# Kernel tuning notes

Hardware: AMD Instinct MI355X
Metric: run time of the kernel (lower is better)

Reference implementation:

```python
import jax, jax.numpy as jnp
import numpy as np

B, S, H, NUM_P = 32, 1024, 768, 49
P2 = NUM_P * 2


def setup_inputs() -> dict:
    key = jax.random.key(0)
    ks = jax.random.split(key, 8)
    hidden_states = jax.random.normal(ks[0], (B, S, H), dtype=jnp.float32)
    batch_subject_ids = jax.random.randint(ks[1], (B, 2), 0, S, dtype=jnp.int32)
    input_mask = jax.random.randint(ks[2], (B, S), 0, 2, dtype=jnp.int32)
    attn_w = jax.random.normal(ks[3], (1, H), dtype=jnp.float32) * 0.02
    attn_b = jnp.zeros((1,), dtype=jnp.float32)
    gate_w = jax.random.normal(ks[4], (H, 2 * H), dtype=jnp.float32) * 0.02
    gate_b = jnp.zeros((H,), dtype=jnp.float32)
    lin_w = jax.random.normal(ks[5], (P2, H), dtype=jnp.float32) * 0.02
    lin_b = jnp.zeros((P2,), dtype=jnp.float32)
    return {
        'hidden_states': hidden_states,
        'batch_subject_ids': batch_subject_ids,
        'input_mask': input_mask,
        'attn_w': attn_w,
        'attn_b': attn_b,
        'gate_w': gate_w,
        'gate_b': gate_b,
        'lin_w': lin_w,
        'lin_b': lin_b,
    }


def reference(hidden_states, batch_subject_ids, input_mask, attn_w, attn_b,
              gate_w, gate_b, lin_w, lin_b):
    # NOTE: the torch module computes s = h[s_start] + h[s_end] from
    # batch_subject_ids but never uses it -> dead code, omitted.
    # Dropout(p=0.4) is treated in eval mode (identity).
    b, s, h = hidden_states.shape
    # cue_len per batch, clamped to [1, S] as in the torch code
    cue_len = jnp.clip(jnp.sum(input_mask, axis=-1), 1, s)            # [B]
    valid = jnp.arange(s)[None, :] < cue_len[:, None]                 # [B,S] bool

    # attention pooling over the first cue_len tokens
    scores = jnp.einsum('bsh,oh->bso', hidden_states, attn_w) + attn_b  # [B,S,1]
    scores = jnp.where(valid[..., None], scores, -jnp.inf)
    attn = jax.nn.softmax(scores, axis=1)                             # [B,S,1]
    s_x = jnp.sum(attn * hidden_states, axis=1)                       # [B,H]

    # gate(cat([s_x, h_i])) split into the two halves of gate_w
    gate_ws = gate_w[:, :h]   # acts on s_x
    gate_wh = gate_w[:, h:]   # acts on h_i
    g_logit = (jnp.einsum('bh,oh->bo', s_x, gate_ws)[:, None, :]
               + jnp.einsum('bsh,oh->bso', hidden_states, gate_wh)
               + gate_b)                                              # [B,S,H]
    g = jax.nn.sigmoid(g_logit)
    fused = g * s_x[:, None, :] + (1.0 - g) * hidden_states           # [B,S,H]
    all_s = jnp.where(valid[..., None], fused, 0.0)                   # zeros beyond cue_len

    hs = hidden_states + all_s
    out = jax.nn.sigmoid(jnp.einsum('bsh,oh->bso', hs, lin_w) + lin_b)
    eps = 1e-7
    return jnp.clip(out, eps, 1.0 - eps)                              # [B,S,2*num_p]
```

## Files before the change

kernel.cpp:

```cpp
#include <hip/hip_runtime.h>
#include <hip/hip_bf16.h>
#include <cstdint>

#define NB 32
#define NS 1024
#define NH 768
#define NP 98

typedef __attribute__((ext_vector_type(8))) short short8;
typedef __attribute__((ext_vector_type(4))) float f32x4;

static __device__ __forceinline__ ushort f2bf(float f) {
  uint32_t u = __builtin_bit_cast(uint32_t, f);
  u += 0x7fff + ((u >> 16) & 1);
  return (ushort)(u >> 16);
}
static __device__ __forceinline__ float bf2f(ushort h) {
  uint32_t u = ((uint32_t)h) << 16;
  return __builtin_bit_cast(float, u);
}
static __device__ __forceinline__ void gload16(const ushort* g, ushort* l) {
  __builtin_amdgcn_global_load_lds((const __attribute__((address_space(1))) uint32_t*)g,
                                   (__attribute__((address_space(3))) uint32_t*)l, 16, 0, 0);
}

__global__ void k_wprep(const float* __restrict__ gate_w, const float* __restrict__ lin_w,
                        ushort* __restrict__ wh_bf, ushort* __restrict__ gs_bf,
                        ushort* __restrict__ lin_bf) {
  int r = blockIdx.x, t = threadIdx.x;
  if (r < NH) {
    float4 v = *(const float4*)(gate_w + (size_t)r * (2 * NH) + NH + t * 4);
    ushort4 h;
    h.x = f2bf(v.x); h.y = f2bf(v.y); h.z = f2bf(v.z); h.w = f2bf(v.w);
    *(ushort4*)&wh_bf[(size_t)r * NH + t * 4] = h;
  } else if (r < 2 * NH) {
    int n = r - NH;
    float4 v = *(const float4*)(gate_w + (size_t)n * (2 * NH) + t * 4);
    ushort4 h;
    h.x = f2bf(v.x); h.y = f2bf(v.y); h.z = f2bf(v.z); h.w = f2bf(v.w);
    *(ushort4*)&gs_bf[(size_t)n * NH + t * 4] = h;
  } else {
    int n = r - 2 * NH;
    ushort4 h; h.x = 0; h.y = 0; h.z = 0; h.w = 0;
    if (n < NP) {
      float4 v = *(const float4*)(lin_w + (size_t)n * NH + t * 4);
      h.x = f2bf(v.x); h.y = f2bf(v.y); h.z = f2bf(v.z); h.w = f2bf(v.w);
    }
    *(ushort4*)&lin_bf[(size_t)n * NH + t * 4] = h;
  }
}

__global__ void k_prep(const float* __restrict__ hidden, const float* __restrict__ aw,
                       const float* __restrict__ ab, ushort* __restrict__ hid_bf,
                       float* __restrict__ scores) {
  int wid = threadIdx.x >> 6, lane = threadIdx.x & 63;
  int rbase = blockIdx.x * 32 + wid * 8;
  float w0[12];
#pragma unroll
  for (int j = 0; j < 3; ++j) {
    float4 wv = *(const float4*)(aw + j * 256 + lane * 4);
    w0[4 * j] = wv.x; w0[4 * j + 1] = wv.y; w0[4 * j + 2] = wv.z; w0[4 * j + 3] = wv.w;
  }
  float abv = ab[0];
  for (int r = rbase; r < rbase + 8; ++r) {
    const float* row = hidden + (size_t)r * NH;
    float acc = 0.f;
#pragma unroll
    for (int j = 0; j < 3; ++j) {
      float4 v = *(const float4*)(row + j * 256 + lane * 4);
      acc += v.x * w0[4 * j] + v.y * w0[4 * j + 1] + v.z * w0[4 * j + 2] + v.w * w0[4 * j + 3];
      ushort4 h;
      h.x = f2bf(v.x); h.y = f2bf(v.y); h.z = f2bf(v.z); h.w = f2bf(v.w);
      *(ushort4*)&hid_bf[(size_t)r * NH + j * 256 + lane * 4] = h;
    }
#pragma unroll
    for (int off = 32; off; off >>= 1) acc += __shfl_xor(acc, off);
    if (lane == 0) scores[r] = acc + abv;
  }
}

__global__ void k_stats(const int* __restrict__ mask, const float* __restrict__ scores,
                        int* __restrict__ cue, float* __restrict__ mout,
                        float* __restrict__ lout) {
  int b = blockIdx.x, t = threadIdx.x;
  int lane = t & 63, w = t >> 6;
  __shared__ float red[4];
  __shared__ int redi[4];
  __shared__ int cue_s;

  int sm = 0;
#pragma unroll
  for (int i = 0; i < 4; ++i) sm += mask[b * NS + t + 256 * i];
#pragma unroll
  for (int off = 32; off; off >>= 1) sm += __shfl_xor(sm, off);
  if (lane == 0) redi[w] = sm;
  __syncthreads();
  if (t == 0) {
    int tot = redi[0] + redi[1] + redi[2] + redi[3];
    tot = min(max(tot, 1), NS);
    cue_s = tot;
    cue[b] = tot;
  }
  __syncthreads();
  int cl = cue_s;

  float mx = -1e30f;
#pragma unroll
  for (int i = 0; i < 4; ++i) {
    int s = t + 256 * i;
    if (s < cl) mx = fmaxf(mx, scores[b * NS + s]);
  }
#pragma unroll
  for (int off = 32; off; off >>= 1) mx = fmaxf(mx, __shfl_xor(mx, off));
  if (lane == 0) red[w] = mx;
  __syncthreads();
  float m = fmaxf(fmaxf(red[0], red[1]), fmaxf(red[2], red[3]));
  __syncthreads();

  float sum = 0.f;
#pragma unroll
  for (int i = 0; i < 4; ++i) {
    int s = t + 256 * i;
    if (s < cl) sum += __expf(scores[b * NS + s] - m);
  }
#pragma unroll
  for (int off = 32; off; off >>= 1) sum += __shfl_xor(sum, off);
  if (lane == 0) red[w] = sum;
  __syncthreads();
  if (t == 0) {
    mout[b] = m;
    lout[b] = red[0] + red[1] + red[2] + red[3];
  }
}

__global__ void k_sx(const ushort* __restrict__ hid_bf, const float* __restrict__ scores,
                     const int* __restrict__ cue, const float* __restrict__ m,
                     const float* __restrict__ l, float* __restrict__ sx) {
  int b = blockIdx.y, ch = blockIdx.x, t = threadIdx.x;
  int s0 = ch * 64;
  int cl = cue[b];
  if (s0 >= cl) return;
  __shared__ float w[64];
  if (t < 64) {
    int s = s0 + t;
    float wv = 0.f;
    if (s < cl) wv = __expf(scores[b * NS + s] - m[b]) / l[b];
    w[t] = wv;
  }
  __syncthreads();
  float4 a; a.x = 0.f; a.y = 0.f; a.z = 0.f; a.w = 0.f;
  const ushort* base = hid_bf + ((size_t)(b * NS + s0)) * NH;
  for (int s = 0; s < 64; ++s) {
    float ws = w[s];
    ushort4 v = *(const ushort4*)(base + s * NH + t * 4);
    a.x = fmaf(ws, bf2f(v.x), a.x);
    a.y = fmaf(ws, bf2f(v.y), a.y);
    a.z = fmaf(ws, bf2f(v.z), a.z);
    a.w = fmaf(ws, bf2f(v.w), a.w);
  }
  float* dst = sx + b * NH + t * 4;
  atomicAdd(dst + 0, a.x);
  atomicAdd(dst + 1, a.y);
  atomicAdd(dst + 2, a.z);
  atomicAdd(dst + 3, a.w);
}

__global__ void k_g1(const float* __restrict__ sx, const ushort* __restrict__ gs_bf,
                     float* __restrict__ g1) {
  int b = blockIdx.y, og = blockIdx.x, t = threadIdx.x;
  int w = t >> 6, lane = t & 63;
  float sreg[12];
#pragma unroll
  for (int e = 0; e < 12; ++e) sreg[e] = sx[b * NH + lane * 12 + e];
#pragma unroll 4
  for (int j = 0; j < 32; ++j) {
    int o = og * 128 + w * 32 + j;
    const ushort* gr = gs_bf + (size_t)o * NH + lane * 12;
    ushort us[12];
    *(ushort4*)&us[0] = *(const ushort4*)(gr);
    *(ushort4*)&us[4] = *(const ushort4*)(gr + 4);
    *(ushort4*)&us[8] = *(const ushort4*)(gr + 8);
    float acc = 0.f;
#pragma unroll
    for (int e = 0; e < 12; ++e) acc = fmaf(bf2f(us[e]), sreg[e], acc);
#pragma unroll
    for (int off = 32; off; off >>= 1) acc += __shfl_xor(acc, off);
    if (lane == 0) g1[b * NH + o] = acc;
  }
}

__global__ __launch_bounds__(256, 3) void k_gemm1(
    const ushort* __restrict__ hid_bf, const ushort* __restrict__ wh_bf,
    const float* __restrict__ gate_b, const float* __restrict__ sx,
    const float* __restrict__ g1, const int* __restrict__ cue,
    ushort* __restrict__ hs_bf) {
  __shared__ ushort As[2][128 * 32];
  __shared__ ushort Bs[2][192 * 32];
  const int t = threadIdx.x;
  const int lane = t & 63, wid = t >> 6;
  const int half = lane >> 4, r16 = lane & 15;

  const int bid = blockIdx.x;
  const int xcd = bid & 7, i = bid >> 3;
  const int nt = i & 3, mt = xcd * 32 + (i >> 2);
  const int row0 = mt * 128, col0 = nt * 192;

  const int c0 = t, c1 = t + 256, c2 = t + 512;
  const ushort* gA0 = hid_bf + (size_t)(row0 + (c0 >> 2)) * NH + (c0 & 3) * 8;
  const ushort* gA1 = hid_bf + (size_t)(row0 + (c1 >> 2)) * NH + (c1 & 3) * 8;
  const ushort* gB0 = wh_bf + (size_t)(col0 + (c0 >> 2)) * NH + (c0 & 3) * 8;
  const ushort* gB1 = wh_bf + (size_t)(col0 + (c1 >> 2)) * NH + (c1 & 3) * 8;
  const ushort* gB2 = wh_bf + (size_t)(col0 + (c2 >> 2)) * NH + (c2 & 3) * 8;

  const int wm = wid >> 1, wn = wid & 1;
  f32x4 acc[4][6];
#pragma unroll
  for (int mf = 0; mf < 4; ++mf)
#pragma unroll
    for (int nf = 0; nf < 6; ++nf) acc[mf][nf] = (f32x4)0.f;

#define STAGE1(BUF, KS)                                  \
  {                                                      \
    const int k0_ = (KS) * 32;                           \
    gload16(gA0 + k0_, &As[BUF][c0 * 8]);                \
    gload16(gA1 + k0_, &As[BUF][c1 * 8]);                \
    gload16(gB0 + k0_, &Bs[BUF][c0 * 8]);                \
    gload16(gB1 + k0_, &Bs[BUF][c1 * 8]);                \
    gload16(gB2 + k0_, &Bs[BUF][c2 * 8]);                \
  }

#define COMPUTE1(BUF)                                                             \
  {                                                                               \
    short8 af[4], bfr[6];                                                         \
    _Pragma("unroll") for (int mf = 0; mf < 4; ++mf)                              \
        af[mf] = *(const short8*)&As[BUF][(wm * 64 + mf * 16 + r16) * 32 + half * 8]; \
    _Pragma("unroll") for (int nf = 0; nf < 6; ++nf)                              \
        bfr[nf] = *(const short8*)&Bs[BUF][(wn * 96 + nf * 16 + r16) * 32 + half * 8]; \
    _Pragma("unroll") for (int nf = 0; nf < 6; ++nf)                              \
        _Pragma("unroll") for (int mf = 0; mf < 4; ++mf)                          \
            acc[mf][nf] = __builtin_amdgcn_mfma_f32_16x16x32_bf16(af[mf], bfr[nf], \
                                                                  acc[mf][nf], 0, 0, 0); \
  }

  STAGE1(0, 0);
  __syncthreads();
#pragma unroll 1
  for (int ks2 = 0; ks2 < 12; ++ks2) {
    const int ks = ks2 * 2;
    STAGE1(1, ks + 1);
    COMPUTE1(0);
    __syncthreads();
    if (ks + 2 < 24) STAGE1(0, ks + 2);
    COMPUTE1(1);
    __syncthreads();
  }

  const int b = mt >> 3;
  const int cl = cue[b];
#pragma unroll
  for (int nf = 0; nf < 6; ++nf) {
    int col = col0 + wn * 96 + nf * 16 + r16;
    float g1v = g1[b * NH + col];
    float sxv = sx[b * NH + col];
    float gbv = gate_b[col];
#pragma unroll
    for (int mf = 0; mf < 4; ++mf) {
#pragma unroll
      for (int p = 0; p < 4; ++p) {
        int grow = row0 + wm * 64 + mf * 16 + half * 4 + p;
        float x = bf2f(hid_bf[(size_t)grow * NH + col]);
        float gl = g1v + acc[mf][nf][p] + gbv;
        float g = 1.f / (1.f + __expf(-gl));
        float fused = g * sxv + (1.f - g) * x;
        float hs = x + (((grow & 1023) < cl) ? fused : 0.f);
        hs_bf[(size_t)grow * NH + col] = f2bf(hs);
      }
    }
  }
#undef STAGE1
#undef COMPUTE1
}

__global__ __launch_bounds__(256, 4) void k_gemm2(
    const ushort* __restrict__ hs_bf, const ushort* __restrict__ lin_bf,
    const float* __restrict__ lin_b, float* __restrict__ out) {
  __shared__ ushort As[2][64 * 32];
  __shared__ ushort Bs[2][128 * 32];
  const int t = threadIdx.x;
  const int lane = t & 63, wid = t >> 6;
  const int half = lane >> 4, r16 = lane & 15;
  const int row0 = blockIdx.x * 64;

  const int cA = t;
  const int cB0 = t, cB1 = t + 256;
  const ushort* gA = hs_bf + (size_t)(row0 + (cA >> 2)) * NH + (cA & 3) * 8;
  const ushort* gB0 = lin_bf + (size_t)(cB0 >> 2) * NH + (cB0 & 3) * 8;
  const ushort* gB1 = lin_bf + (size_t)(cB1 >> 2) * NH + (cB1 & 3) * 8;

  f32x4 acc[7];
#pragma unroll
  for (int nf = 0; nf < 7; ++nf) acc[nf] = (f32x4)0.f;

#define STAGE2(BUF, KS)                                  \
  {                                                      \
    const int k0_ = (KS) * 32;                           \
    gload16(gA + k0_, &As[BUF][cA * 8]);                 \
    gload16(gB0 + k0_, &Bs[BUF][cB0 * 8]);               \
    gload16(gB1 + k0_, &Bs[BUF][cB1 * 8]);               \
  }

#define COMPUTE2(BUF)                                                          \
  {                                                                            \
    short8 a = *(const short8*)&As[BUF][(wid * 16 + r16) * 32 + half * 8];     \
    _Pragma("unroll") for (int nf = 0; nf < 7; ++nf) {                         \
      short8 bv = *(const short8*)&Bs[BUF][(nf * 16 + r16) * 32 + half * 8];   \
      acc[nf] = __builtin_amdgcn_mfma_f32_16x16x32_bf16(a, bv, acc[nf], 0, 0, 0); \
    }                                                                          \
  }

  STAGE2(0, 0);
  __syncthreads();
#pragma unroll 1
  for (int ks2 = 0; ks2 < 12; ++ks2) {
    const int ks = ks2 * 2;
    STAGE2(1, ks + 1);
    COMPUTE2(0);
    __syncthreads();
    if (ks + 2 < 24) STAGE2(0, ks + 2);
    COMPUTE2(1);
    __syncthreads();
  }

#pragma unroll
  for (int nf = 0; nf < 7; ++nf) {
    int col = nf * 16 + r16;
    bool valid = col < NP;
    float lbv = valid ? lin_b[col] : 0.f;
#pragma unroll
    for (int p = 0; p < 4; ++p) {
      int grow = row0 + wid * 16 + half * 4 + p;
      float v = acc[nf][p] + lbv;
      v = 1.f / (1.f + __expf(-v));
      v = fminf(fmaxf(v, 1e-7f), 1.f - 1e-7f);
      if (valid) out[(size_t)grow * NP + col] = v;
    }
  }
#undef STAGE2
#undef COMPUTE2
}

extern "C" void kernel_launch(void* const* d_in, const int* in_sizes, int n_in,
                              void* d_out, int out_size, void* d_ws, size_t ws_size,
                              hipStream_t stream) {
  const float* hidden = (const float*)d_in[0];
  const int* mask = (const int*)d_in[2];
  const float* attn_w = (const float*)d_in[3];
  const float* attn_b = (const float*)d_in[4];
  const float* gate_w = (const float*)d_in[5];
  const float* gate_b = (const float*)d_in[6];
  const float* lin_w = (const float*)d_in[7];
  const float* lin_b = (const float*)d_in[8];
  float* out = (float*)d_out;

  float* F = (float*)d_ws;
  int* cue = (int*)F;
  float* m = F + 32;
  float* l = F + 64;
  float* scores = F + 96;
  float* sx = scores + NB * NS;
  float* g1 = sx + NB * NH;
  ushort* wh_bf = (ushort*)(g1 + NB * NH);
  ushort* gs_bf = wh_bf + (size_t)NH * NH;
  ushort* lin_bf = gs_bf + (size_t)NH * NH;
  ushort* hid_bf = lin_bf + (size_t)128 * NH;
  ushort* hs_bf = hid_bf + (size_t)NB * NS * NH;

  hipMemsetAsync(sx, 0, NB * NH * sizeof(float), stream);
  k_wprep<<<1664, 192, 0, stream>>>(gate_w, lin_w, wh_bf, gs_bf, lin_bf);
  k_prep<<<1024, 256, 0, stream>>>(hidden, attn_w, attn_b, hid_bf, scores);
  k_stats<<<NB, 256, 0, stream>>>(mask, scores, cue, m, l);
  k_sx<<<dim3(16, NB), 192, 0, stream>>>(hid_bf, scores, cue, m, l, sx);
  k_g1<<<dim3(6, NB), 256, 0, stream>>>(sx, gs_bf, g1);
  k_gemm1<<<1024, 256, 0, stream>>>(hid_bf, wh_bf, gate_b, sx, g1, cue, hs_bf);
  k_gemm2<<<512, 256, 0, stream>>>(hs_bf, lin_bf, lin_b, out);
}
```

Baseline: 344.7 us.

## Triple-buffer GEMM pipelines with swizzled LDS and retile gemm1 to 128x128

Both GEMM kernels move from double-buffered loads with two __syncthreads per pair of k-steps to a three-stage LDS ring. Each step issues a single explicit vmcnt wait plus barrier, so global-to-LDS loads run two stages ahead of the MFMA work. An XOR swizzle on the k-quad offset is applied to both the global-load addresses and the LDS fragment reads to cut bank conflicts. gemm1 is retiled from 128x192 to 128x128 with a 1536-block grid, which lowers accumulator registers but reloads A more often. The hand-written waitcnt counts must match the number of in-flight loads exactly or the results will be wrong.

```diff
diff --git a/kernel.cpp b/kernel.cpp
--- a/kernel.cpp
+++ b/kernel.cpp
@@ -194,72 +194,79 @@
     const float* __restrict__ gate_b, const float* __restrict__ sx,
     const float* __restrict__ g1, const int* __restrict__ cue,
     ushort* __restrict__ hs_bf) {
-  __shared__ ushort As[2][128 * 32];
-  __shared__ ushort Bs[2][192 * 32];
+  __shared__ ushort As[3][128 * 32];
+  __shared__ ushort Bs[3][128 * 32];
   const int t = threadIdx.x;
   const int lane = t & 63, wid = t >> 6;
   const int half = lane >> 4, r16 = lane & 15;
 
   const int bid = blockIdx.x;
   const int xcd = bid & 7, i = bid >> 3;
-  const int nt = i & 3, mt = xcd * 32 + (i >> 2);
-  const int row0 = mt * 128, col0 = nt * 192;
-
-  const int c0 = t, c1 = t + 256, c2 = t + 512;
-  const ushort* gA0 = hid_bf + (size_t)(row0 + (c0 >> 2)) * NH + (c0 & 3) * 8;
-  const ushort* gA1 = hid_bf + (size_t)(row0 + (c1 >> 2)) * NH + (c1 & 3) * 8;
-  const ushort* gB0 = wh_bf + (size_t)(col0 + (c0 >> 2)) * NH + (c0 & 3) * 8;
-  const ushort* gB1 = wh_bf + (size_t)(col0 + (c1 >> 2)) * NH + (c1 & 3) * 8;
-  const ushort* gB2 = wh_bf + (size_t)(col0 + (c2 >> 2)) * NH + (c2 & 3) * 8;
+  const int nt = i % 6, mt = xcd * 32 + i / 6;
+  const int row0 = mt * 128, col0 = nt * 128;
+
+  const int xs = ((t >> 2) & 3) ^ ((t >> 4) & 3);
+  const int kqs = ((t & 3) ^ xs) * 8;
+  const ushort* gA0 = hid_bf + (size_t)(row0 + (t >> 2)) * NH + kqs;
+  const ushort* gA1 = hid_bf + (size_t)(row0 + 64 + (t >> 2)) * NH + kqs;
+  const ushort* gB0 = wh_bf + (size_t)(col0 + (t >> 2)) * NH + kqs;
+  const ushort* gB1 = wh_bf + (size_t)(col0 + 64 + (t >> 2)) * NH + kqs;
+  const int xr = (r16 & 3) ^ ((r16 >> 2) & 3);
 
   const int wm = wid >> 1, wn = wid & 1;
-  f32x4 acc[4][6];
+  f32x4 acc[4][4];
 #pragma unroll
   for (int mf = 0; mf < 4; ++mf)
 #pragma unroll
-    for (int nf = 0; nf < 6; ++nf) acc[mf][nf] = (f32x4)0.f;
-
-#define STAGE1(BUF, KS)                                  \
-  {                                                      \
-    const int k0_ = (KS) * 32;                           \
-    gload16(gA0 + k0_, &As[BUF][c0 * 8]);                \
-    gload16(gA1 + k0_, &As[BUF][c1 * 8]);                \
-    gload16(gB0 + k0_, &Bs[BUF][c0 * 8]);                \
-    gload16(gB1 + k0_, &Bs[BUF][c1 * 8]);                \
-    gload16(gB2 + k0_, &Bs[BUF][c2 * 8]);                \
-  }
-
-#define COMPUTE1(BUF)                                                             \
-  {                                                                               \
-    short8 af[4], bfr[6];                                                         \
-    _Pragma("unroll") for (int mf = 0; mf < 4; ++mf)                              \
-        af[mf] = *(const short8*)&As[BUF][(wm * 64 + mf * 16 + r16) * 32 + half * 8]; \
-    _Pragma("unroll") for (int nf = 0; nf < 6; ++nf)                              \
-        bfr[nf] = *(const short8*)&Bs[BUF][(wn * 96 + nf * 16 + r16) * 32 + half * 8]; \
-    _Pragma("unroll") for (int nf = 0; nf < 6; ++nf)                              \
-        _Pragma("unroll") for (int mf = 0; mf < 4; ++mf)                          \
-            acc[mf][nf] = __builtin_amdgcn_mfma_f32_16x16x32_bf16(af[mf], bfr[nf], \
+    for (int nf = 0; nf < 4; ++nf) acc[mf][nf] = (f32x4)0.f;
+
+#define STAGE1(BUF, KS)                                   \
+  {                                                       \
+    const int k0_ = (KS) * 32;                            \
+    gload16(gA0 + k0_, &As[BUF][t * 8]);                  \
+    gload16(gA1 + k0_, &As[BUF][(t + 256) * 8]);          \
+    gload16(gB0 + k0_, &Bs[BUF][t * 8]);                  \
+    gload16(gB1 + k0_, &Bs[BUF][(t + 256) * 8]);          \
+  }
+
+#define COMPUTE1(BUF)                                                               \
+  {                                                                                 \
+    short8 af[4], bfr[4];                                                           \
+    _Pragma("unroll") for (int mf = 0; mf < 4; ++mf)                                \
+        af[mf] = *(const short8*)&As[BUF][(wm * 64 + mf * 16 + r16) * 32 +          \
+                                          ((half ^ xr) * 8)];                       \
+    _Pragma("unroll") for (int nf = 0; nf < 4; ++nf)                                \
+        bfr[nf] = *(const short8*)&Bs[BUF][(wn * 64 + nf * 16 + r16) * 32 +         \
+                                           ((half ^ xr) * 8)];                      \
+    _Pragma("unroll") for (int nf = 0; nf < 4; ++nf)                                \
+        _Pragma("unroll") for (int mf = 0; mf < 4; ++mf)                            \
+            acc[mf][nf] = __builtin_amdgcn_mfma_f32_16x16x32_bf16(af[mf], bfr[nf],  \
                                                                   acc[mf][nf], 0, 0, 0); \
   }
 
+#define WAITBAR(N)                                       \
+  asm volatile("s_waitcnt vmcnt(" #N ")" ::: "memory");  \
+  __builtin_amdgcn_s_barrier();                          \
+  __builtin_amdgcn_sched_barrier(0);
+
   STAGE1(0, 0);
-  __syncthreads();
+  STAGE1(1, 1);
 #pragma unroll 1
-  for (int ks2 = 0; ks2 < 12; ++ks2) {
-    const int ks = ks2 * 2;
-    STAGE1(1, ks + 1);
-    COMPUTE1(0);
-    __syncthreads();
-    if (ks + 2 < 24) STAGE1(0, ks + 2);
-    COMPUTE1(1);
-    __syncthreads();
-  }
+  for (int tt = 0; tt < 7; ++tt) {
+    const int s0_ = tt * 3;
+    WAITBAR(4); COMPUTE1(0); STAGE1(2, s0_ + 2);
+    WAITBAR(4); COMPUTE1(1); STAGE1(0, s0_ + 3);
+    WAITBAR(4); COMPUTE1(2); STAGE1(1, s0_ + 4);
+  }
+  WAITBAR(4); COMPUTE1(0); STAGE1(2, 23);
+  WAITBAR(4); COMPUTE1(1);
+  WAITBAR(0); COMPUTE1(2);
 
   const int b = mt >> 3;
   const int cl = cue[b];
 #pragma unroll
-  for (int nf = 0; nf < 6; ++nf) {
-    int col = col0 + wn * 96 + nf * 16 + r16;
+  for (int nf = 0; nf < 4; ++nf) {
+    int col = col0 + wn * 64 + nf * 16 + r16;
     float g1v = g1[b * NH + col];
     float sxv = sx[b * NH + col];
     float gbv = gate_b[col];
@@ -284,55 +291,61 @@
 __global__ __launch_bounds__(256, 4) void k_gemm2(
     const ushort* __restrict__ hs_bf, const ushort* __restrict__ lin_bf,
     const float* __restrict__ lin_b, float* __restrict__ out) {
-  __shared__ ushort As[2][64 * 32];
-  __shared__ ushort Bs[2][128 * 32];
+  __shared__ ushort As[3][64 * 32];
+  __shared__ ushort Bs[3][128 * 32];
   const int t = threadIdx.x;
   const int lane = t & 63, wid = t >> 6;
   const int half = lane >> 4, r16 = lane & 15;
   const int row0 = blockIdx.x * 64;
 
-  const int cA = t;
-  const int cB0 = t, cB1 = t + 256;
-  const ushort* gA = hs_bf + (size_t)(row0 + (cA >> 2)) * NH + (cA & 3) * 8;
-  const ushort* gB0 = lin_bf + (size_t)(cB0 >> 2) * NH + (cB0 & 3) * 8;
-  const ushort* gB1 = lin_bf + (size_t)(cB1 >> 2) * NH + (cB1 & 3) * 8;
-
-  f32x4 acc[7];
-#pragma unroll
-  for (int nf = 0; nf < 7; ++nf) acc[nf] = (f32x4)0.f;
-
-#define STAGE2(BUF, KS)                                  \
-  {                                                      \
-    const int k0_ = (KS) * 32;                           \
-    gload16(gA + k0_, &As[BUF][cA * 8]);                 \
-    gload16(gB0 + k0_, &Bs[BUF][cB0 * 8]);               \
-    gload16(gB1 + k0_, &Bs[BUF][cB1 * 8]);               \
-  }
-
-#define COMPUTE2(BUF)                                                          \
-  {                                                                            \
-    short8 a = *(const short8*)&As[BUF][(wid * 16 + r16) * 32 + half * 8];     \
-    _Pragma("unroll") for (int nf = 0; nf < 7; ++nf) {                         \
-      short8 bv = *(const short8*)&Bs[BUF][(nf * 16 + r16) * 32 + half * 8];   \
-      acc[nf] = __builtin_amdgcn_mfma_f32_16x16x32_bf16(a, bv, acc[nf], 0, 0, 0); \
-    }                                                                          \
-  }
+  const int xs = ((t >> 2) & 3) ^ ((t >> 4) & 3);
+  const int kqs = ((t & 3) ^ xs) * 8;
+  const ushort* gA = hs_bf + (size_t)(row0 + (t >> 2)) * NH + kqs;
+  const ushort* gB0 = lin_bf + (size_t)(t >> 2) * NH + kqs;
+  const ushort* gB1 = lin_bf + (size_t)(64 + (t >> 2)) * NH + kqs;
+  const int xr = (r16 & 3) ^ ((r16 >> 2) & 3);
+
+  f32x4 acc[8];
+#pragma unroll
+  for (int nf = 0; nf < 8; ++nf) acc[nf] = (f32x4)0.f;
+
+#define STAGE2(BUF, KS)                                   \
+  {                                                       \
+    const int k0_ = (KS) * 32;                            \
+    gload16(gA + k0_, &As[BUF][t * 8]);                   \
+    gload16(gB0 + k0_, &Bs[BUF][t * 8]);                  \
+    gload16(gB1 + k0_, &Bs[BUF][(t + 256) * 8]);          \
+  }
+
+#define COMPUTE2(BUF)                                                               \
+  {                                                                                 \
+    short8 a = *(const short8*)&As[BUF][(wid * 16 + r16) * 32 + ((half ^ xr) * 8)]; \
+    _Pragma("unroll") for (int nf = 0; nf < 8; ++nf) {                              \
+      short8 bv = *(const short8*)&Bs[BUF][(nf * 16 + r16) * 32 + ((half ^ xr) * 8)]; \
+      acc[nf] = __builtin_amdgcn_mfma_f32_16x16x32_bf16(a, bv, acc[nf], 0, 0, 0);   \
+    }                                                                               \
+  }
+
+#define WAITBAR2(N)                                      \
+  asm volatile("s_waitcnt vmcnt(" #N ")" ::: "memory");  \
+  __builtin_amdgcn_s_barrier();                          \
+  __builtin_amdgcn_sched_barrier(0);
 
   STAGE2(0, 0);
-  __syncthreads();
+  STAGE2(1, 1);
 #pragma unroll 1
-  for (int ks2 = 0; ks2 < 12; ++ks2) {
-    const int ks = ks2 * 2;
-    STAGE2(1, ks + 1);
-    COMPUTE2(0);
-    __syncthreads();
-    if (ks + 2 < 24) STAGE2(0, ks + 2);
-    COMPUTE2(1);
-    __syncthreads();
-  }
-
-#pragma unroll
-  for (int nf = 0; nf < 7; ++nf) {
+  for (int tt = 0; tt < 7; ++tt) {
+    const int s0_ = tt * 3;
+    WAITBAR2(3); COMPUTE2(0); STAGE2(2, s0_ + 2);
+    WAITBAR2(3); COMPUTE2(1); STAGE2(0, s0_ + 3);
+    WAITBAR2(3); COMPUTE2(2); STAGE2(1, s0_ + 4);
+  }
+  WAITBAR2(3); COMPUTE2(0); STAGE2(2, 23);
+  WAITBAR2(3); COMPUTE2(1);
+  WAITBAR2(0); COMPUTE2(2);
+
+#pragma unroll
+  for (int nf = 0; nf < 8; ++nf) {
     int col = nf * 16 + r16;
     bool valid = col < NP;
     float lbv = valid ? lin_b[col] : 0.f;
@@ -347,6 +360,7 @@
   }
 #undef STAGE2
 #undef COMPUTE2
+#undef WAITBAR2
 }
 
 extern "C" void kernel_launch(void* const* d_in, const int* in_sizes, int n_in,
@@ -381,6 +395,6 @@
   k_stats<<<NB, 256, 0, stream>>>(mask, scores, cue, m, l);
   k_sx<<<dim3(16, NB), 192, 0, stream>>>(hid_bf, scores, cue, m, l, sx);
   k_g1<<<dim3(6, NB), 256, 0, stream>>>(sx, gs_bf, g1);
-  k_gemm1<<<1024, 256, 0, stream>>>(hid_bf, wh_bf, gate_b, sx, g1, cue, hs_bf);
+  k_gemm1<<<1536, 256, 0, stream>>>(hid_bf, wh_bf, gate_b, sx, g1, cue, hs_bf);
   k_gemm2<<<512, 256, 0, stream>>>(hs_bf, lin_bf, lin_b, out);
 }
```

Result: faster. 290.4 us (-15.7%).
